# Optimization experiments

Hardware: AMD Instinct MI355X
Metric: run time of the kernel (lower is better)

The kernel has to match this reference:

```python
import jax, jax.numpy as jnp
import numpy as np

B, MAX_NODE, MEM_LEN, DIM, HEADS, LAYERS, DEG = 32, 1024, 256, 128, 4, 4, 16
CH = DIM // HEADS


def setup_inputs() -> dict:
    key = jax.random.key(0)
    ks = jax.random.split(key, 16)
    counts = np.array([512 + 16 * i for i in range(B)])  # ragged graph sizes, sum = 24320
    N = int(counts.sum())
    node2batch = np.repeat(np.arange(B), counts)
    node2pos = np.concatenate([np.arange(c) for c in counts])
    bmask = np.arange(MAX_NODE)[None, :] < counts[:, None]
    rng = np.random.default_rng(0)
    srcs, dsts, off = [], [], 0
    for c in counts:  # edges stay within each graph
        srcs.append(off + rng.integers(0, c, size=DEG * c))
        dsts.append(off + rng.integers(0, c, size=DEG * c))
        off += c
    edge_index = np.stack([np.concatenate(srcs), np.concatenate(dsts)])

    def rn(k, shape, scale=0.05):
        return jax.random.normal(k, shape, jnp.float32) * scale

    return dict(
        node_feats=rn(ks[0], (N, DIM), 1.0),
        edge_feats=rn(ks[1], (edge_index.shape[1], DIM), 1.0),
        memory=rn(ks[2], (B, MEM_LEN, DIM), 1.0),
        Wn=rn(ks[3], (LAYERS, DIM, DIM)), bn=jnp.zeros((LAYERS, DIM)),
        We=rn(ks[4], (LAYERS, DIM, DIM)),
        att_src=rn(ks[5], (LAYERS, HEADS, CH)),
        att_dst=rn(ks[6], (LAYERS, HEADS, CH)),
        att_edge=rn(ks[7], (LAYERS, HEADS, CH)),
        ln1_g=jnp.ones((LAYERS, DIM)), ln1_b=jnp.zeros((LAYERS, DIM)),
        ln2_g=jnp.ones((LAYERS, DIM)), ln2_b=jnp.zeros((LAYERS, DIM)),
        Wq=rn(ks[8], (LAYERS, DIM, DIM)), Wk=rn(ks[9], (LAYERS, DIM, DIM)),
        Wv=rn(ks[10], (LAYERS, DIM, DIM)), Wo=rn(ks[11], (LAYERS, DIM, DIM)),
        Ew1=rn(ks[12], (LAYERS, 3 * DIM, DIM)), Eb1=jnp.zeros((LAYERS, DIM)),
        Ew2=rn(ks[13], (LAYERS, DIM, DIM)), Eb2=jnp.zeros((LAYERS, DIM)),
        edge_index=jnp.asarray(edge_index, jnp.int32),
        node2batch=jnp.asarray(node2batch, jnp.int32),
        node2pos=jnp.asarray(node2pos, jnp.int32),
        batch_mask=jnp.asarray(bmask),
        mem_pad_mask=jnp.ones((B, MEM_LEN), bool),
    )


def _ln(x, g, b):
    mu = x.mean(-1, keepdims=True)
    v = ((x - mu) ** 2).mean(-1, keepdims=True)
    return (x - mu) * jax.lax.rsqrt(v + 1e-5) * g + b


def reference(node_feats, edge_feats, memory, Wn, bn, We, att_src, att_dst, att_edge,
              ln1_g, ln1_b, ln2_g, ln2_b, Wq, Wk, Wv, Wo, Ew1, Eb1, Ew2, Eb2,
              edge_index, node2batch, node2pos, batch_mask, mem_pad_mask):
    N = node_feats.shape[0]
    src, dst = edge_index[0], edge_index[1]
    # [B, max_node, mem_len]: attend only valid memory slots from valid nodes
    cross_mask = mem_pad_mask[:, None, :] & batch_mask[:, :, None]
    x, e = node_feats, edge_feats
    for l in range(LAYERS):
        # --- edge-conditioned GAT conv (segment softmax over dst) ---
        h = (x @ Wn[l]).reshape(N, HEADS, CH)
        eh = (e @ We[l]).reshape(-1, HEADS, CH)
        logits = (h[src] * att_src[l]).sum(-1) + (h[dst] * att_dst[l]).sum(-1) + (eh * att_edge[l]).sum(-1)
        logits = jax.nn.leaky_relu(logits, 0.2)  # [E, H]
        m = jax.ops.segment_max(logits, dst, num_segments=N)
        ew = jnp.exp(logits - m[dst])
        den = jax.ops.segment_sum(ew, dst, num_segments=N)
        alpha = ew / (den[dst] + 1e-16)
        conv = jax.ops.segment_sum(alpha[..., None] * (h[src] + eh), dst, num_segments=N)
        conv = conv.reshape(N, DIM) + bn[l]
        x = jax.nn.relu(_ln(conv, ln1_g[l], ln1_b[l])) + x
        # --- graph2batch scatter into dense padded tensor ---
        dense = jnp.zeros((B, MAX_NODE, DIM), x.dtype).at[node2batch, node2pos].set(x)
        # --- cross attention against memory ---
        q = (dense @ Wq[l]).reshape(B, MAX_NODE, HEADS, CH)
        k = (memory @ Wk[l]).reshape(B, MEM_LEN, HEADS, CH)
        v = (memory @ Wv[l]).reshape(B, MEM_LEN, HEADS, CH)
        scores = jnp.einsum('bqhc,bkhc->bhqk', q, k) / np.float32(np.sqrt(CH))
        scores = jnp.where(cross_mask[:, None], scores, jnp.float32(-1e9))
        ao = jnp.einsum('bhqk,bkhc->bqhc', jax.nn.softmax(scores, axis=-1), v)
        ao = ao.reshape(B, MAX_NODE, DIM) @ Wo[l]
        dense = jax.nn.relu(_ln(ao + dense, ln2_g[l], ln2_b[l]))
        x = dense[node2batch, node2pos]  # batch2graph gather
        # --- residual sparse edge update ---
        ecat = jnp.concatenate([e, x[src], x[dst]], axis=-1)
        e = e + jax.nn.relu(ecat @ Ew1[l] + Eb1[l]) @ Ew2[l] + Eb2[l]
    return x, e
```

## Files before the change

kernel.cpp:

```cpp
#include <hip/hip_runtime.h>

#define DIM    128
#define HEADS  4
#define CH     32
#define MEMLEN 256
#define LAYERS 4

typedef unsigned int uint;
typedef unsigned short ushort;
using bf16x8 = __attribute__((ext_vector_type(8))) short;
using f32x4  = __attribute__((ext_vector_type(4))) float;

__device__ __forceinline__ ushort bf16_rn(float x) {
    uint u = __float_as_uint(x);
    uint r = (u + 0x7fffu + ((u >> 16) & 1u)) >> 16;
    return (ushort)r;
}
__device__ __forceinline__ void split_bf(float v, ushort& h, ushort& lo) {
    h = bf16_rn(v);
    float hf = __uint_as_float(((uint)h) << 16);
    lo = bf16_rn(v - hf);
}


__global__ void copy_f4(const float4* __restrict__ in, float4* __restrict__ out, long n) {
    long i = (long)blockIdx.x * blockDim.x + threadIdx.x;
    long stride = (long)gridDim.x * blockDim.x;
    for (; i < n; i += stride) out[i] = in[i];
}

__global__ void hist_k(const int* __restrict__ dst, int E, int* __restrict__ deg) {
    int e = blockIdx.x * blockDim.x + threadIdx.x;
    if (e < E) atomicAdd(&deg[dst[e]], 1);
}

__global__ void csr_offsets(const int* __restrict__ deg, int n, int* __restrict__ off) {
    __shared__ int part[1024];
    int t = threadIdx.x;
    int chunk = (n + 1023) >> 10;
    int lo = t * chunk, hi = min(lo + chunk, n);
    int s = 0;
    for (int i = lo; i < hi; i++) s += deg[i];
    part[t] = s; __syncthreads();
    for (int d = 1; d < 1024; d <<= 1) {
        int v = part[t];
        int add = (t >= d) ? part[t - d] : 0;
        __syncthreads();
        part[t] = v + add;
        __syncthreads();
    }
    int run = (t == 0) ? 0 : part[t - 1];
    for (int i = lo; i < hi; i++) { off[i] = run; run += deg[i]; }
    if (t == 1023) off[n] = part[1023];
}

__global__ void csr_fill(const int* __restrict__ dst, int E, const int* __restrict__ off,
                         int* __restrict__ cur, int* __restrict__ csr) {
    int e = blockIdx.x * blockDim.x + threadIdx.x;
    if (e < E) {
        int d = dst[e];
        int p = atomicAdd(&cur[d], 1);
        csr[off[d] + p] = e;
    }
}

__global__ void make_w1f(const float* __restrict__ Ew1, ushort* __restrict__ W1f) {
    int i = blockIdx.x * 256 + threadIdx.x;
    if (i >= LAYERS * 12 * 8 * 64 * 8) return;
    int l = i / 49152; int r = i % 49152;
    int ks = r / 4096;  int r2 = r % 4096;
    int ct = r2 / 512;  int r3 = r2 % 512;
    int lane = r3 / 8;  int j = r3 % 8;
    int k = ks * 32 + (lane >> 4) * 8 + j;
    int n = (lane & 15) + 16 * ct;
    const float* W = Ew1 + (size_t)l * 3 * DIM * DIM;
    float v = W[(size_t)(k % 128) * DIM + n];
    ushort h = bf16_rn(v);
    ushort out = h;
    if (k >= 256) {
        float hf = __uint_as_float(((uint)h) << 16);
        out = bf16_rn(v - hf);
    }
    W1f[i] = out;
}

__global__ void make_w2f(const float* __restrict__ Ew2, ushort* __restrict__ W2f) {
    int i = blockIdx.x * 256 + threadIdx.x;
    if (i >= LAYERS * 8 * 8 * 64 * 8) return;
    int l = i / 32768; int r = i % 32768;
    int ks = r / 4096;  int r2 = r % 4096;
    int ct = r2 / 512;  int r3 = r2 % 512;
    int lane = r3 / 8;  int j = r3 % 8;
    int k = ks * 32 + (lane >> 4) * 8 + j;
    int n = (lane & 15) + 16 * ct;
    const float* W = Ew2 + (size_t)l * DIM * DIM;
    W2f[i] = bf16_rn(W[(size_t)(k >> 1) * DIM + n]);
}

__global__ __launch_bounds__(256) void gemm128(const float* __restrict__ A,
                                               const float* __restrict__ W,
                                               const float* __restrict__ bias,
                                               float* __restrict__ out, int R) {
    int r0 = blockIdx.x * 64, t = threadIdx.x;
    __shared__ float at[64][DIM];
    for (int i = t; i < 64 * 32; i += 256) {
        int rr = i >> 5, cc = i & 31;
        if (r0 + rr < R)
            ((float4*)at[rr])[cc] = ((const float4*)(A + (size_t)(r0 + rr) * DIM))[cc];
    }
    __syncthreads();
    int c0 = (t & 31) * 4;
    int rb = (t >> 5) * 8;
    float acc[8][4];
#pragma unroll
    for (int ee = 0; ee < 8; ee++)
        acc[ee][0] = acc[ee][1] = acc[ee][2] = acc[ee][3] = 0.f;
    for (int k = 0; k < DIM; k += 4) {
        float4 w0 = *(const float4*)&W[(k + 0) * DIM + c0];
        float4 w1 = *(const float4*)&W[(k + 1) * DIM + c0];
        float4 w2 = *(const float4*)&W[(k + 2) * DIM + c0];
        float4 w3 = *(const float4*)&W[(k + 3) * DIM + c0];
#pragma unroll
        for (int ee = 0; ee < 8; ee++) {
            float4 a = *(float4*)&at[rb + ee][k];
            acc[ee][0] += a.x * w0.x + a.y * w1.x + a.z * w2.x + a.w * w3.x;
            acc[ee][1] += a.x * w0.y + a.y * w1.y + a.z * w2.y + a.w * w3.y;
            acc[ee][2] += a.x * w0.z + a.y * w1.z + a.z * w2.z + a.w * w3.z;
            acc[ee][3] += a.x * w0.w + a.y * w1.w + a.z * w2.w + a.w * w3.w;
        }
    }
    float4 bb = make_float4(0.f, 0.f, 0.f, 0.f);
    if (bias) bb = *(const float4*)&bias[c0];
#pragma unroll
    for (int ee = 0; ee < 8; ee++) {
        int r = r0 + rb + ee;
        if (r < R) {
            float4 o = make_float4(acc[ee][0] + bb.x, acc[ee][1] + bb.y,
                                   acc[ee][2] + bb.z, acc[ee][3] + bb.w);
            *(float4*)&out[(size_t)r * DIM + c0] = o;
        }
    }
}

__global__ __launch_bounds__(256, 2) void gemm128_dual(const float* __restrict__ A,
                                                       const float* __restrict__ Wa,
                                                       const float* __restrict__ Wb,
                                                       const float* __restrict__ biasA,
                                                       float* __restrict__ outA,
                                                       float* __restrict__ outB, int R) {
    int r0 = blockIdx.x * 64, t = threadIdx.x;
    __shared__ float at[64][DIM];
    for (int i = t; i < 64 * 32; i += 256) {
        int rr = i >> 5, cc = i & 31;
        if (r0 + rr < R)
            ((float4*)at[rr])[cc] = ((const float4*)(A + (size_t)(r0 + rr) * DIM))[cc];
    }
    __syncthreads();
    int c0 = (t & 31) * 4;
    int rb = (t >> 5) * 8;
    float accA[8][4], accB[8][4];
#pragma unroll
    for (int ee = 0; ee < 8; ee++)
#pragma unroll
        for (int j = 0; j < 4; j++) { accA[ee][j] = 0.f; accB[ee][j] = 0.f; }
    for (int k = 0; k < DIM; k += 4) {
        float4 wa0 = *(const float4*)&Wa[(k + 0) * DIM + c0];
        float4 wa1 = *(const float4*)&Wa[(k + 1) * DIM + c0];
        float4 wa2 = *(const float4*)&Wa[(k + 2) * DIM + c0];
        float4 wa3 = *(const float4*)&Wa[(k + 3) * DIM + c0];
        float4 wb0 = *(const float4*)&Wb[(k + 0) * DIM + c0];
        float4 wb1 = *(const float4*)&Wb[(k + 1) * DIM + c0];
        float4 wb2 = *(const float4*)&Wb[(k + 2) * DIM + c0];
        float4 wb3 = *(const float4*)&Wb[(k + 3) * DIM + c0];
#pragma unroll
        for (int ee = 0; ee < 8; ee++) {
            float4 a = *(float4*)&at[rb + ee][k];
            accA[ee][0] += a.x * wa0.x + a.y * wa1.x + a.z * wa2.x + a.w * wa3.x;
            accA[ee][1] += a.x * wa0.y + a.y * wa1.y + a.z * wa2.y + a.w * wa3.y;
            accA[ee][2] += a.x * wa0.z + a.y * wa1.z + a.z * wa2.z + a.w * wa3.z;
            accA[ee][3] += a.x * wa0.w + a.y * wa1.w + a.z * wa2.w + a.w * wa3.w;
            accB[ee][0] += a.x * wb0.x + a.y * wb1.x + a.z * wb2.x + a.w * wb3.x;
            accB[ee][1] += a.x * wb0.y + a.y * wb1.y + a.z * wb2.y + a.w * wb3.y;
            accB[ee][2] += a.x * wb0.z + a.y * wb1.z + a.z * wb2.z + a.w * wb3.z;
            accB[ee][3] += a.x * wb0.w + a.y * wb1.w + a.z * wb2.w + a.w * wb3.w;
        }
    }
    float4 bb = make_float4(0.f, 0.f, 0.f, 0.f);
    if (biasA) bb = *(const float4*)&biasA[c0];
#pragma unroll
    for (int ee = 0; ee < 8; ee++) {
        int r = r0 + rb + ee;
        if (r < R) {
            *(float4*)&outA[(size_t)r * DIM + c0] =
                make_float4(accA[ee][0] + bb.x, accA[ee][1] + bb.y,
                            accA[ee][2] + bb.z, accA[ee][3] + bb.w);
            *(float4*)&outB[(size_t)r * DIM + c0] =
                make_float4(accB[ee][0], accB[ee][1], accB[ee][2], accB[ee][3]);
        }
    }
}

__global__ __launch_bounds__(256) void node_proj_tile(
    const float* __restrict__ x, const float* __restrict__ W,
    const float* __restrict__ att_s, const float* __restrict__ att_d,
    float* __restrict__ h, float* __restrict__ ssrc, float* __restrict__ sdst, int N) {
    int r0 = blockIdx.x * 64, t = threadIdx.x;
    __shared__ float at[64][DIM];
    for (int i = t; i < 64 * 32; i += 256) {
        int rr = i >> 5, cc = i & 31;
        if (r0 + rr < N)
            ((float4*)at[rr])[cc] = ((const float4*)(x + (size_t)(r0 + rr) * DIM))[cc];
    }
    __syncthreads();
    int c0 = (t & 31) * 4;
    int rb = (t >> 5) * 8;
    float acc[8][4];
#pragma unroll
    for (int ee = 0; ee < 8; ee++)
        acc[ee][0] = acc[ee][1] = acc[ee][2] = acc[ee][3] = 0.f;
    for (int k = 0; k < DIM; k += 4) {
        float4 w0 = *(const float4*)&W[(k + 0) * DIM + c0];
        float4 w1 = *(const float4*)&W[(k + 1) * DIM + c0];
        float4 w2 = *(const float4*)&W[(k + 2) * DIM + c0];
        float4 w3 = *(const float4*)&W[(k + 3) * DIM + c0];
#pragma unroll
        for (int ee = 0; ee < 8; ee++) {
            float4 a = *(float4*)&at[rb + ee][k];
            acc[ee][0] += a.x * w0.x + a.y * w1.x + a.z * w2.x + a.w * w3.x;
            acc[ee][1] += a.x * w0.y + a.y * w1.y + a.z * w2.y + a.w * w3.y;
            acc[ee][2] += a.x * w0.z + a.y * w1.z + a.z * w2.z + a.w * w3.z;
            acc[ee][3] += a.x * w0.w + a.y * w1.w + a.z * w2.w + a.w * w3.w;
        }
    }
    int hh = (t & 31) >> 3;
    float4 as = *(const float4*)&att_s[c0];
    float4 ad = *(const float4*)&att_d[c0];
#pragma unroll
    for (int ee = 0; ee < 8; ee++) {
        int r = r0 + rb + ee;
        if (r < N) {
            *(float4*)&h[(size_t)r * DIM + c0] =
                make_float4(acc[ee][0], acc[ee][1], acc[ee][2], acc[ee][3]);
            float ps = acc[ee][0]*as.x + acc[ee][1]*as.y + acc[ee][2]*as.z + acc[ee][3]*as.w;
            float pd = acc[ee][0]*ad.x + acc[ee][1]*ad.y + acc[ee][2]*ad.z + acc[ee][3]*ad.w;
#pragma unroll
            for (int mk = 1; mk < 8; mk <<= 1) {
                ps += __shfl_xor(ps, mk, 32);
                pd += __shfl_xor(pd, mk, 32);
            }
            if (((t & 31) & 7) == 0) {
                ssrc[r * HEADS + hh] = ps;
                sdst[r * HEADS + hh] = pd;
            }
        }
    }
}


__global__ void make_waE(const float* __restrict__ We, const float* __restrict__ att_e,
                         float* __restrict__ waE) {
    int k = threadIdx.x;
#pragma unroll
    for (int h = 0; h < HEADS; h++) {
        float s = 0.f;
#pragma unroll
        for (int c = 0; c < CH; c++) s += We[k * DIM + h * CH + c] * att_e[h * CH + c];
        waE[k * HEADS + h] = s;
    }
}

__global__ void sedge_logits(const float* __restrict__ e, const float* __restrict__ waE,
                             const float* __restrict__ ssrc, const float* __restrict__ sdst,
                             const int* __restrict__ src, const int* __restrict__ dst,
                             float* __restrict__ lw, int E) {
    __shared__ float w[DIM * HEADS];
    int t = threadIdx.x;
    w[t] = waE[t]; w[t + 256] = waE[t + 256];
    __syncthreads();
    int g = t >> 5, lane = t & 31;
    int eid = blockIdx.x * 8 + g;
    if (eid >= E) return;
    const float* er = e + (size_t)eid * DIM;
    float s0 = 0.f, s1 = 0.f, s2 = 0.f, s3 = 0.f;
#pragma unroll
    for (int j = 0; j < 4; j++) {
        int k = lane + 32 * j;
        float v = er[k];
        s0 += v * w[k * 4 + 0]; s1 += v * w[k * 4 + 1];
        s2 += v * w[k * 4 + 2]; s3 += v * w[k * 4 + 3];
    }
#pragma unroll
    for (int m = 16; m; m >>= 1) {
        s0 += __shfl_xor(s0, m, 32); s1 += __shfl_xor(s1, m, 32);
        s2 += __shfl_xor(s2, m, 32); s3 += __shfl_xor(s3, m, 32);
    }
    if (lane == 0) {
        int sn = src[eid] * HEADS, dn = dst[eid] * HEADS;
        float l0 = ssrc[sn + 0] + sdst[dn + 0] + s0;
        float l1 = ssrc[sn + 1] + sdst[dn + 1] + s1;
        float l2 = ssrc[sn + 2] + sdst[dn + 2] + s2;
        float l3 = ssrc[sn + 3] + sdst[dn + 3] + s3;
        lw[eid * 4 + 0] = (l0 >= 0.f) ? l0 : 0.2f * l0;
        lw[eid * 4 + 1] = (l1 >= 0.f) ? l1 : 0.2f * l1;
        lw[eid * 4 + 2] = (l2 >= 0.f) ? l2 : 0.2f * l2;
        lw[eid * 4 + 3] = (l3 >= 0.f) ? l3 : 0.2f * l3;
    }
}

__global__ void seg_softmax(const int* __restrict__ off, const int* __restrict__ csr,
                            float* __restrict__ lw, float* __restrict__ den, int NH) {
    int i = blockIdx.x * blockDim.x + threadIdx.x;
    if (i >= NH) return;
    int n = i >> 2, hh = i & 3;
    int o0 = off[n], o1 = off[n + 1];
    float m = -1e30f;
    for (int o = o0; o < o1; o++) m = fmaxf(m, lw[csr[o] * HEADS + hh]);
    float s = 0.f;
    for (int o = o0; o < o1; o++) {
        int idx = csr[o] * HEADS + hh;
        float w = __expf(lw[idx] - m);
        lw[idx] = w;
        s += w;
    }
    den[i] = s;
}

__global__ __launch_bounds__(512) void conv_ln4(
    const int* __restrict__ off, const int* __restrict__ csr, const int* __restrict__ src,
    const float* __restrict__ lw, const float* __restrict__ den,
    const float* __restrict__ hbuf, const float* __restrict__ e, const float* __restrict__ We,
    const float* __restrict__ bn, const float* __restrict__ g, const float* __restrict__ b,
    float* __restrict__ x, int N) {
    int t = threadIdx.x;
    int tt = t & 127, part = t >> 7;
    int n = blockIdx.x;
    int hh = tt >> 5;
    __shared__ float aggeP[4][HEADS][DIM];
    __shared__ float acchP[4][DIM];
    __shared__ float ehcP[4][DIM];
    __shared__ float wred[16];
    int o0 = off[n], o1 = off[n + 1];
    float acch = 0.f, a0 = 0.f, a1 = 0.f, a2 = 0.f, a3 = 0.f;
    for (int o = o0 + part; o < o1; o += 4) {
        int eid = csr[o];
        int s = src[eid];
        float4 al = *(const float4*)&lw[eid * 4];
        acch += ((&al.x)[hh]) * hbuf[(size_t)s * DIM + tt];
        float ev = e[(size_t)eid * DIM + tt];
        a0 += al.x * ev; a1 += al.y * ev; a2 += al.z * ev; a3 += al.w * ev;
    }
    aggeP[part][0][tt] = a0; aggeP[part][1][tt] = a1;
    aggeP[part][2][tt] = a2; aggeP[part][3][tt] = a3;
    acchP[part][tt] = acch;
    __syncthreads();
    float ehc = 0.f;
    int k0 = part * 32;
    for (int k = k0; k < k0 + 32; k++) {
        float ag = aggeP[0][hh][k] + aggeP[1][hh][k] + aggeP[2][hh][k] + aggeP[3][hh][k];
        ehc += ag * We[k * DIM + tt];
    }
    ehcP[part][tt] = ehc;
    __syncthreads();
    float conv = (acchP[0][tt] + acchP[1][tt] + acchP[2][tt] + acchP[3][tt]
                + ehcP[0][tt] + ehcP[1][tt] + ehcP[2][tt] + ehcP[3][tt])
                 / (den[n * HEADS + hh] + 1e-16f) + bn[tt];
    int w = t >> 6;
    float s1 = conv;
#pragma unroll
    for (int mk = 32; mk; mk >>= 1) s1 += __shfl_xor(s1, mk, 64);
    if ((t & 63) == 0) wred[w] = s1;
    __syncthreads();
    float mu = (wred[w] + wred[w ^ 1]) * (1.f / DIM);
    float diff = conv - mu;
    float s2 = diff * diff;
#pragma unroll
    for (int mk = 32; mk; mk >>= 1) s2 += __shfl_xor(s2, mk, 64);
    if ((t & 63) == 0) wred[8 + w] = s2;
    __syncthreads();
    float var = (wred[8 + w] + wred[8 + (w ^ 1)]) * (1.f / DIM);
    if (part == 0) {
        float y = diff * rsqrtf(var + 1e-5f) * g[tt] + b[tt];
        x[(size_t)n * DIM + tt] = fmaxf(y, 0.f) + x[(size_t)n * DIM + tt];
    }
}

__global__ __launch_bounds__(256) void cross_attn_tile(
    float* __restrict__ x, const float* __restrict__ qg,
    const float* __restrict__ kb, const float* __restrict__ vb,
    const float* __restrict__ Wo, const float* __restrict__ g,
    const float* __restrict__ b, const int* __restrict__ boff) {
    int bb = blockIdx.y;
    int n0 = boff[bb] + blockIdx.x * 64;
    int cnt = boff[bb + 1] - n0;
    if (cnt <= 0) return;
    int nq = min(64, cnt);
    int t = threadIdx.x;
    int q = t & 63, h = t >> 6;

    __shared__ float smem[64 * 132];

    float qv[32];
    if (q < nq) {
        const float4* qp = (const float4*)(qg + (size_t)(n0 + q) * DIM + h * CH);
#pragma unroll
        for (int j = 0; j < 8; j++) {
            float4 v = qp[j];
            qv[4*j+0] = v.x; qv[4*j+1] = v.y; qv[4*j+2] = v.z; qv[4*j+3] = v.w;
        }
    } else {
#pragma unroll
        for (int c = 0; c < 32; c++) qv[c] = 0.f;
    }

    float oacc[32];
#pragma unroll
    for (int c = 0; c < 32; c++) oacc[c] = 0.f;
    float m = -1e30f, l = 0.f;

    const float4* Ksrc = (const float4*)(kb + (size_t)bb * MEMLEN * DIM);
    const float4* Vsrc = (const float4*)(vb + (size_t)bb * MEMLEN * DIM);
    float4* Kl = (float4*)smem;
    float4* Vl = (float4*)(smem + 32 * DIM);

    for (int ch = 0; ch < MEMLEN / 32; ch++) {
        __syncthreads();
#pragma unroll
        for (int r = 0; r < 4; r++) {
            int idx = t + r * 256;
            Kl[idx] = Ksrc[ch * 1024 + idx];
            Vl[idx] = Vsrc[ch * 1024 + idx];
        }
        __syncthreads();
        float sc[32];
#pragma unroll
        for (int kk = 0; kk < 32; kk++) {
            const float* kp = smem + kk * DIM + h * CH;
            float s = 0.f;
#pragma unroll
            for (int c = 0; c < 32; c++) s += qv[c] * kp[c];
            sc[kk] = s * 0.17677669529663689f;
        }
        float mc = sc[0];
#pragma unroll
        for (int kk = 1; kk < 32; kk++) mc = fmaxf(mc, sc[kk]);
        float mn = fmaxf(m, mc);
        float scale = __expf(m - mn);
        m = mn;
        float ls = 0.f;
#pragma unroll
        for (int kk = 0; kk < 32; kk++) {
            float w = __expf(sc[kk] - mn);
            sc[kk] = w;
            ls += w;
        }
        l = l * scale + ls;
#pragma unroll
        for (int c = 0; c < 32; c++) oacc[c] *= scale;
#pragma unroll
        for (int kk = 0; kk < 32; kk++) {
            const float* vp = smem + 32 * DIM + kk * DIM + h * CH;
            float w = sc[kk];
#pragma unroll
            for (int c = 0; c < 32; c++) oacc[c] += w * vp[c];
        }
    }
    __syncthreads();
    {
        float inv = 1.f / l;
        float* ap = smem + q * 132 + h * CH;
#pragma unroll
        for (int c = 0; c < 32; c++) ap[c] = oacc[c] * inv;
    }
    __syncthreads();
    int c0 = (t & 31) * 4;
    int rb = (t >> 5) * 8;
    float acc2[8][4];
#pragma unroll
    for (int ee = 0; ee < 8; ee++)
        acc2[ee][0] = acc2[ee][1] = acc2[ee][2] = acc2[ee][3] = 0.f;
    for (int k = 0; k < DIM; k += 4) {
        float4 w0 = *(const float4*)&Wo[(k + 0) * DIM + c0];
        float4 w1 = *(const float4*)&Wo[(k + 1) * DIM + c0];
        float4 w2 = *(const float4*)&Wo[(k + 2) * DIM + c0];
        float4 w3 = *(const float4*)&Wo[(k + 3) * DIM + c0];
#pragma unroll
        for (int ee = 0; ee < 8; ee++) {
            float4 a = *(const float4*)(smem + (rb + ee) * 132 + k);
            acc2[ee][0] += a.x * w0.x + a.y * w1.x + a.z * w2.x + a.w * w3.x;
            acc2[ee][1] += a.x * w0.y + a.y * w1.y + a.z * w2.y + a.w * w3.y;
            acc2[ee][2] += a.x * w0.z + a.y * w1.z + a.z * w2.z + a.w * w3.z;
            acc2[ee][3] += a.x * w0.w + a.y * w1.w + a.z * w2.w + a.w * w3.w;
        }
    }
    float4 gg = *(const float4*)&g[c0];
    float4 bb4 = *(const float4*)&b[c0];
#pragma unroll
    for (int ee = 0; ee < 8; ee++) {
        int r = rb + ee;
        if (r < nq) {
            float4 xr = *(const float4*)&x[(size_t)(n0 + r) * DIM + c0];
            float o0 = acc2[ee][0] + xr.x, o1 = acc2[ee][1] + xr.y;
            float o2 = acc2[ee][2] + xr.z, o3 = acc2[ee][3] + xr.w;
            float s1 = o0 + o1 + o2 + o3;
#pragma unroll
            for (int mk = 16; mk; mk >>= 1) s1 += __shfl_xor(s1, mk, 32);
            float mu = s1 * (1.f / DIM);
            float d0 = o0 - mu, d1 = o1 - mu, d2 = o2 - mu, d3 = o3 - mu;
            float s2 = d0*d0 + d1*d1 + d2*d2 + d3*d3;
#pragma unroll
            for (int mk = 16; mk; mk >>= 1) s2 += __shfl_xor(s2, mk, 32);
            float rs = rsqrtf(s2 * (1.f / DIM) + 1e-5f);
            float4 o = make_float4(fmaxf(d0 * rs * gg.x + bb4.x, 0.f),
                                   fmaxf(d1 * rs * gg.y + bb4.y, 0.f),
                                   fmaxf(d2 * rs * gg.z + bb4.z, 0.f),
                                   fmaxf(d3 * rs * gg.w + bb4.w, 0.f));
            *(float4*)&x[(size_t)(n0 + r) * DIM + c0] = o;
        }
    }
}

__global__ __launch_bounds__(256) void edge_mlp_mfma(
    float* __restrict__ e, const float* __restrict__ xs, const float* __restrict__ xd,
    const int* __restrict__ src, const int* __restrict__ dst,
    const ushort* __restrict__ W1f,
    const ushort* __restrict__ W2f,
    const float* __restrict__ Eb2, int E) {
    __shared__ ushort As[64 * 256];
    __shared__ ushort Bs[2][4096];
    int t = threadIdx.x;
    int e0 = blockIdx.x * 64;

#pragma unroll
    for (int it = 0; it < 8; it++) {
        int i = t + it * 256;
        int row = i >> 5, c4 = i & 31;
        float4 v;
        if (e0 + row < E) v = *(const float4*)&e[(size_t)(e0 + row) * DIM + c4 * 4];
        else v = make_float4(0.f, 0.f, 0.f, 0.f);
        ushort h0, l0, h1, l1, h2, l2, h3, l3;
        split_bf(v.x, h0, l0); split_bf(v.y, h1, l1);
        split_bf(v.z, h2, l2); split_bf(v.w, h3, l3);
        int k = c4 * 4;
        int off = k & 7;
        int kbh = (k >> 3) ^ (row & 7);
        int kbl = ((128 + k) >> 3) ^ (row & 7);
        uint2 hw, lw2;
        hw.x = (uint)h0 | ((uint)h1 << 16); hw.y = (uint)h2 | ((uint)h3 << 16);
        lw2.x = (uint)l0 | ((uint)l1 << 16); lw2.y = (uint)l2 | ((uint)l3 << 16);
        *(uint2*)&As[row * 256 + kbh * 8 + off] = hw;
        *(uint2*)&As[row * 256 + kbl * 8 + off] = lw2;
    }

    auto loadB = [&](const ushort* Wf, int ks, uint4& p0, uint4& p1) {
        const ushort* s = Wf + (size_t)ks * 4096;
        p0 = *(const uint4*)&s[t * 8];
        p1 = *(const uint4*)&s[(t + 256) * 8];
    };
    auto writeB = [&](int buf, const uint4& p0, const uint4& p1) {
        *(uint4*)&Bs[buf][t * 8] = p0;
        *(uint4*)&Bs[buf][(t + 256) * 8] = p1;
    };

    {
        uint4 p0, p1;
        loadB(W1f, 0, p0, p1);
        writeB(0, p0, p1);
    }
    __syncthreads();

    int l = t & 63, wid = t >> 6;
    int rowbase = wid * 16;
    int arow = rowbase + (l & 15);
    int g = l >> 4;
    int swz = arow & 7;

    f32x4 acc[8];
#pragma unroll
    for (int ct = 0; ct < 8; ct++) acc[ct] = (f32x4){0.f, 0.f, 0.f, 0.f};

    for (int ks = 0; ks < 12; ks++) {
        int buf = ks & 1;
        uint4 p0, p1;
        bool havepf = (ks + 1) < 12;
        if (havepf) loadB(W1f, ks + 1, p0, p1);
        int ksA = (ks < 8) ? ks : (ks - 8);
        int kbm = (ksA * 4 + g) ^ swz;
        bf16x8 af = *(bf16x8*)&As[arow * 256 + kbm * 8];
#pragma unroll
        for (int ct = 0; ct < 8; ct++) {
            bf16x8 bfrag = *(bf16x8*)&Bs[buf][(ct * 64 + l) * 8];
            acc[ct] = __builtin_amdgcn_mfma_f32_16x16x32_bf16(af, bfrag, acc[ct], 0, 0, 0);
        }
        __syncthreads();
        if (havepf) writeB(buf ^ 1, p0, p1);
        __syncthreads();
    }

    int srow[4], drow[4], grow4[4];
#pragma unroll
    for (int j = 0; j < 4; j++) {
        int grow = e0 + rowbase + g * 4 + j;
        grow4[j] = grow;
        if (grow < E) { srow[j] = src[grow]; drow[j] = dst[grow]; }
        else { srow[j] = 0; drow[j] = 0; }
    }
#pragma unroll
    for (int ct = 0; ct < 8; ct++) {
        int col = (l & 15) + 16 * ct;
        int kb = col >> 2;
        int off = (2 * col) & 7;
#pragma unroll
        for (int j = 0; j < 4; j++) {
            float v = acc[ct][j];
            if (grow4[j] < E)
                v += xs[(size_t)srow[j] * DIM + col] + xd[(size_t)drow[j] * DIM + col];
            v = fmaxf(v, 0.f);
            ushort h, lo;
            split_bf(v, h, lo);
            int rowloc = rowbase + g * 4 + j;
            int kbm = kb ^ (rowloc & 7);
            *(uint*)&As[rowloc * 256 + kbm * 8 + off] = (uint)h | ((uint)lo << 16);
        }
    }
    {
        uint4 p0, p1;
        loadB(W2f, 0, p0, p1);
        __syncthreads();
        writeB(0, p0, p1);
    }
    __syncthreads();

    f32x4 acc2[8];
#pragma unroll
    for (int ct = 0; ct < 8; ct++) acc2[ct] = (f32x4){0.f, 0.f, 0.f, 0.f};
    for (int ks = 0; ks < 8; ks++) {
        int buf = ks & 1;
        uint4 p0, p1;
        bool havepf = (ks + 1) < 8;
        if (havepf) loadB(W2f, ks + 1, p0, p1);
        int kbm = (ks * 4 + g) ^ swz;
        bf16x8 af = *(bf16x8*)&As[arow * 256 + kbm * 8];
#pragma unroll
        for (int ct = 0; ct < 8; ct++) {
            bf16x8 bfrag = *(bf16x8*)&Bs[buf][(ct * 64 + l) * 8];
            acc2[ct] = __builtin_amdgcn_mfma_f32_16x16x32_bf16(af, bfrag, acc2[ct], 0, 0, 0);
        }
        __syncthreads();
        if (havepf) writeB(buf ^ 1, p0, p1);
        __syncthreads();
    }

#pragma unroll
    for (int ct = 0; ct < 8; ct++) {
        int col = (l & 15) + 16 * ct;
        float b2 = Eb2[col];
#pragma unroll
        for (int j = 0; j < 4; j++) {
            if (grow4[j] < E) {
                size_t idx = (size_t)grow4[j] * DIM + col;
                e[idx] += acc2[ct][j] + b2;
            }
        }
    }
}


extern "C" void kernel_launch(void* const* d_in, const int* in_sizes, int n_in,
                              void* d_out, int out_size, void* d_ws, size_t ws_size,
                              hipStream_t stream) {
    const float* node_feats = (const float*)d_in[0];
    const float* edge_feats = (const float*)d_in[1];
    const float* memory     = (const float*)d_in[2];
    const float* Wn   = (const float*)d_in[3];
    const float* bn   = (const float*)d_in[4];
    const float* We   = (const float*)d_in[5];
    const float* att_src  = (const float*)d_in[6];
    const float* att_dst  = (const float*)d_in[7];
    const float* att_edge = (const float*)d_in[8];
    const float* ln1_g = (const float*)d_in[9];
    const float* ln1_b = (const float*)d_in[10];
    const float* ln2_g = (const float*)d_in[11];
    const float* ln2_b = (const float*)d_in[12];
    const float* Wq = (const float*)d_in[13];
    const float* Wk = (const float*)d_in[14];
    const float* Wv = (const float*)d_in[15];
    const float* Wo = (const float*)d_in[16];
    const float* Ew1 = (const float*)d_in[17];
    const float* Eb1 = (const float*)d_in[18];
    const float* Ew2 = (const float*)d_in[19];
    const float* Eb2 = (const float*)d_in[20];
    const int* edge_index = (const int*)d_in[21];
    const int* node2batch = (const int*)d_in[22];

    const int N = in_sizes[0] / DIM;
    const int E = in_sizes[1] / DIM;
    const int Bn = in_sizes[2] / (MEMLEN * DIM);
    const int* srcA = edge_index;
    const int* dstA = edge_index + E;

    float* x = (float*)d_out;
    float* e = x + (size_t)N * DIM;

    char* p = (char*)d_ws;
    auto carve = [&](size_t bytes) {
        void* r = (void*)p;
        p += (bytes + 255) & ~(size_t)255;
        return r;
    };
    float* h     = (float*)carve((size_t)N * DIM * 4);
    float* qg    = (float*)carve((size_t)N * DIM * 4);
    float* xs    = (float*)carve((size_t)N * DIM * 4);
    float* xd    = (float*)carve((size_t)N * DIM * 4);
    float* ssrc  = (float*)carve((size_t)N * HEADS * 4);
    float* sdst  = (float*)carve((size_t)N * HEADS * 4);
    float* lw    = (float*)carve((size_t)E * HEADS * 4);
    float* den   = (float*)carve((size_t)N * HEADS * 4);
    float* waE   = (float*)carve((size_t)DIM * HEADS * 4);
    float* kbuf  = (float*)carve((size_t)Bn * MEMLEN * DIM * 4);
    float* vbuf  = (float*)carve((size_t)Bn * MEMLEN * DIM * 4);
    ushort* W1f  = (ushort*)carve((size_t)LAYERS * 12 * 4096 * 2);
    ushort* W2f  = (ushort*)carve((size_t)LAYERS * 8 * 4096 * 2);
    int* deg     = (int*)carve((size_t)N * 4);
    int* cur     = (int*)carve((size_t)N * 4);
    int* off     = (int*)carve(((size_t)N + 1) * 4);
    int* csr     = (int*)carve((size_t)E * 4);
    int* bcnt    = (int*)carve((size_t)Bn * 4);
    int* boff    = (int*)carve(((size_t)Bn + 1) * 4);

    {
        long nx = (long)N * DIM / 4;
        copy_f4<<<dim3(2048), dim3(256), 0, stream>>>((const float4*)node_feats, (float4*)x, nx);
        long nen = (long)E * DIM / 4;
        copy_f4<<<dim3(4096), dim3(256), 0, stream>>>((const float4*)edge_feats, (float4*)e, nen);
    }

    make_w1f<<<dim3((LAYERS * 49152 + 255) / 256), dim3(256), 0, stream>>>(Ew1, W1f);
    make_w2f<<<dim3((LAYERS * 32768 + 255) / 256), dim3(256), 0, stream>>>(Ew2, W2f);

    hipMemsetAsync(deg, 0, (size_t)N * 4, stream);
    hipMemsetAsync(cur, 0, (size_t)N * 4, stream);
    hipMemsetAsync(bcnt, 0, (size_t)Bn * 4, stream);
    hist_k<<<dim3((E + 255) / 256), dim3(256), 0, stream>>>(dstA, E, deg);
    csr_offsets<<<dim3(1), dim3(1024), 0, stream>>>(deg, N, off);
    csr_fill<<<dim3((E + 255) / 256), dim3(256), 0, stream>>>(dstA, E, off, cur, csr);
    hist_k<<<dim3((N + 255) / 256), dim3(256), 0, stream>>>(node2batch, N, bcnt);
    csr_offsets<<<dim3(1), dim3(1024), 0, stream>>>(bcnt, Bn, boff);

    const int mrows = Bn * MEMLEN;
    const int maxTiles = 1024 / 64;
    for (int l = 0; l < LAYERS; l++) {
        const float* Wn_l  = Wn  + (size_t)l * DIM * DIM;
        const float* We_l  = We  + (size_t)l * DIM * DIM;
        const float* Wq_l  = Wq  + (size_t)l * DIM * DIM;
        const float* Wo_l  = Wo  + (size_t)l * DIM * DIM;
        const float* Wk_l  = Wk  + (size_t)l * DIM * DIM;
        const float* Wv_l  = Wv  + (size_t)l * DIM * DIM;
        const float* Ew1_l = Ew1 + (size_t)l * 3 * DIM * DIM;

        node_proj_tile<<<dim3((N + 63) / 64), dim3(256), 0, stream>>>(
            x, Wn_l, att_src + l * DIM, att_dst + l * DIM, h, ssrc, sdst, N);
        make_waE<<<dim3(1), dim3(DIM), 0, stream>>>(We_l, att_edge + l * DIM, waE);
        sedge_logits<<<dim3((E + 7) / 8), dim3(256), 0, stream>>>(
            e, waE, ssrc, sdst, srcA, dstA, lw, E);
        seg_softmax<<<dim3((N * HEADS + 255) / 256), dim3(256), 0, stream>>>(
            off, csr, lw, den, N * HEADS);
        conv_ln4<<<dim3(N), dim3(512), 0, stream>>>(
            off, csr, srcA, lw, den, h, e, We_l,
            bn + l * DIM, ln1_g + l * DIM, ln1_b + l * DIM, x, N);
        gemm128_dual<<<dim3((mrows + 63) / 64), dim3(256), 0, stream>>>(
            memory, Wk_l, Wv_l, nullptr, kbuf, vbuf, mrows);
        gemm128<<<dim3((N + 63) / 64), dim3(256), 0, stream>>>(
            x, Wq_l, nullptr, qg, N);
        cross_attn_tile<<<dim3(maxTiles, Bn), dim3(256), 0, stream>>>(
            x, qg, kbuf, vbuf, Wo_l, ln2_g + l * DIM, ln2_b + l * DIM, boff);
        gemm128_dual<<<dim3((N + 63) / 64), dim3(256), 0, stream>>>(
            x, Ew1_l + (size_t)DIM * DIM, Ew1_l + (size_t)2 * DIM * DIM,
            Eb1 + l * DIM, xs, xd, N);
        edge_mlp_mfma<<<dim3((E + 63) / 64), dim3(256), 0, stream>>>(
            e, xs, xd, srcA, dstA,
            W1f + (size_t)l * 12 * 4096, W2f + (size_t)l * 8 * 4096,
            Eb2 + l * DIM, E);
    }
}
```

Before: 3.856 ms.

## Keep edge-MLP weight fragments in registers and split waves by output columns

The edge MLP kernel no longer stages W1/W2 tiles through a double-buffered shared-memory buffer with two barriers per k-step. Each wave now owns two 16-column output tiles across all 64 rows and loads its weight fragments straight from global memory into registers. Only the A operand stays in LDS, and a launch-bounds hint of two blocks per CU is added. This removes the per-step barriers and the LDS traffic for B, in exchange for four times more A-fragment LDS reads per wave and high register pressure from the held fragments, which could cause spills or lower occupancy.

```diff
diff --git a/kernel.cpp b/kernel.cpp
--- a/kernel.cpp
+++ b/kernel.cpp
@@ -519,14 +519,13 @@
     }
 }
 
-__global__ __launch_bounds__(256) void edge_mlp_mfma(
+__global__ __launch_bounds__(256, 2) void edge_mlp_mfma(
     float* __restrict__ e, const float* __restrict__ xs, const float* __restrict__ xd,
     const int* __restrict__ src, const int* __restrict__ dst,
     const ushort* __restrict__ W1f,
     const ushort* __restrict__ W2f,
     const float* __restrict__ Eb2, int E) {
     __shared__ ushort As[64 * 256];
-    __shared__ ushort Bs[2][4096];
     int t = threadIdx.x;
     int e0 = blockIdx.x * 64;
 
@@ -551,114 +550,100 @@
         *(uint2*)&As[row * 256 + kbl * 8 + off] = lw2;
     }
 
-    auto loadB = [&](const ushort* Wf, int ks, uint4& p0, uint4& p1) {
-        const ushort* s = Wf + (size_t)ks * 4096;
-        p0 = *(const uint4*)&s[t * 8];
-        p1 = *(const uint4*)&s[(t + 256) * 8];
-    };
-    auto writeB = [&](int buf, const uint4& p0, const uint4& p1) {
-        *(uint4*)&Bs[buf][t * 8] = p0;
-        *(uint4*)&Bs[buf][(t + 256) * 8] = p1;
-    };
-
-    {
-        uint4 p0, p1;
-        loadB(W1f, 0, p0, p1);
-        writeB(0, p0, p1);
-    }
-    __syncthreads();
-
     int l = t & 63, wid = t >> 6;
-    int rowbase = wid * 16;
-    int arow = rowbase + (l & 15);
     int g = l >> 4;
-    int swz = arow & 7;
-
-    f32x4 acc[8];
-#pragma unroll
-    for (int ct = 0; ct < 8; ct++) acc[ct] = (f32x4){0.f, 0.f, 0.f, 0.f};
-
+    int lr = l & 15;
+    int ct0 = 2 * wid, ct1 = 2 * wid + 1;
+
+    bf16x8 b1[12][2];
+#pragma unroll
     for (int ks = 0; ks < 12; ks++) {
-        int buf = ks & 1;
-        uint4 p0, p1;
-        bool havepf = (ks + 1) < 12;
-        if (havepf) loadB(W1f, ks + 1, p0, p1);
+        b1[ks][0] = *(const bf16x8*)&W1f[(size_t)ks * 4096 + ct0 * 512 + l * 8];
+        b1[ks][1] = *(const bf16x8*)&W1f[(size_t)ks * 4096 + ct1 * 512 + l * 8];
+    }
+
+    __syncthreads();
+
+    f32x4 acc[4][2];
+#pragma unroll
+    for (int r = 0; r < 4; r++) {
+        acc[r][0] = (f32x4){0.f, 0.f, 0.f, 0.f};
+        acc[r][1] = (f32x4){0.f, 0.f, 0.f, 0.f};
+    }
+
+#pragma unroll
+    for (int ks = 0; ks < 12; ks++) {
         int ksA = (ks < 8) ? ks : (ks - 8);
-        int kbm = (ksA * 4 + g) ^ swz;
-        bf16x8 af = *(bf16x8*)&As[arow * 256 + kbm * 8];
-#pragma unroll
-        for (int ct = 0; ct < 8; ct++) {
-            bf16x8 bfrag = *(bf16x8*)&Bs[buf][(ct * 64 + l) * 8];
-            acc[ct] = __builtin_amdgcn_mfma_f32_16x16x32_bf16(af, bfrag, acc[ct], 0, 0, 0);
-        }
-        __syncthreads();
-        if (havepf) writeB(buf ^ 1, p0, p1);
-        __syncthreads();
-    }
-
-    int srow[4], drow[4], grow4[4];
-#pragma unroll
-    for (int j = 0; j < 4; j++) {
-        int grow = e0 + rowbase + g * 4 + j;
-        grow4[j] = grow;
-        if (grow < E) { srow[j] = src[grow]; drow[j] = dst[grow]; }
-        else { srow[j] = 0; drow[j] = 0; }
-    }
-#pragma unroll
-    for (int ct = 0; ct < 8; ct++) {
-        int col = (l & 15) + 16 * ct;
-        int kb = col >> 2;
-        int off = (2 * col) & 7;
+#pragma unroll
+        for (int r = 0; r < 4; r++) {
+            int arow = r * 16 + lr;
+            int kbm = (ksA * 4 + g) ^ (arow & 7);
+            bf16x8 af = *(bf16x8*)&As[arow * 256 + kbm * 8];
+            acc[r][0] = __builtin_amdgcn_mfma_f32_16x16x32_bf16(af, b1[ks][0], acc[r][0], 0, 0, 0);
+            acc[r][1] = __builtin_amdgcn_mfma_f32_16x16x32_bf16(af, b1[ks][1], acc[r][1], 0, 0, 0);
+        }
+    }
+
+    bf16x8 b2f[8][2];
+#pragma unroll
+    for (int ks = 0; ks < 8; ks++) {
+        b2f[ks][0] = *(const bf16x8*)&W2f[(size_t)ks * 4096 + ct0 * 512 + l * 8];
+        b2f[ks][1] = *(const bf16x8*)&W2f[(size_t)ks * 4096 + ct1 * 512 + l * 8];
+    }
+
+    int col0 = lr + 16 * ct0, col1 = lr + 16 * ct1;
+    int kb0 = col0 >> 2, off0 = (2 * col0) & 7;
+    int kb1 = col1 >> 2, off1 = (2 * col1) & 7;
+#pragma unroll
+    for (int r = 0; r < 4; r++) {
 #pragma unroll
         for (int j = 0; j < 4; j++) {
-            float v = acc[ct][j];
-            if (grow4[j] < E)
-                v += xs[(size_t)srow[j] * DIM + col] + xd[(size_t)drow[j] * DIM + col];
-            v = fmaxf(v, 0.f);
-            ushort h, lo;
-            split_bf(v, h, lo);
-            int rowloc = rowbase + g * 4 + j;
-            int kbm = kb ^ (rowloc & 7);
-            *(uint*)&As[rowloc * 256 + kbm * 8 + off] = (uint)h | ((uint)lo << 16);
-        }
-    }
-    {
-        uint4 p0, p1;
-        loadB(W2f, 0, p0, p1);
-        __syncthreads();
-        writeB(0, p0, p1);
-    }
-    __syncthreads();
-
-    f32x4 acc2[8];
-#pragma unroll
-    for (int ct = 0; ct < 8; ct++) acc2[ct] = (f32x4){0.f, 0.f, 0.f, 0.f};
+            int rowloc = r * 16 + g * 4 + j;
+            int grow = e0 + rowloc;
+            float v0 = acc[r][0][j], v1 = acc[r][1][j];
+            if (grow < E) {
+                int s = src[grow], d = dst[grow];
+                v0 += xs[(size_t)s * DIM + col0] + xd[(size_t)d * DIM + col0];
+                v1 += xs[(size_t)s * DIM + col1] + xd[(size_t)d * DIM + col1];
+            }
+            v0 = fmaxf(v0, 0.f); v1 = fmaxf(v1, 0.f);
+            ushort h0s, l0s, h1s, l1s;
+            split_bf(v0, h0s, l0s);
+            split_bf(v1, h1s, l1s);
+            int rs = rowloc & 7;
+            *(uint*)&As[rowloc * 256 + (kb0 ^ rs) * 8 + off0] = (uint)h0s | ((uint)l0s << 16);
+            *(uint*)&As[rowloc * 256 + (kb1 ^ rs) * 8 + off1] = (uint)h1s | ((uint)l1s << 16);
+        }
+    }
+    __syncthreads();
+
+    f32x4 acc2[4][2];
+#pragma unroll
+    for (int r = 0; r < 4; r++) {
+        acc2[r][0] = (f32x4){0.f, 0.f, 0.f, 0.f};
+        acc2[r][1] = (f32x4){0.f, 0.f, 0.f, 0.f};
+    }
+#pragma unroll
     for (int ks = 0; ks < 8; ks++) {
-        int buf = ks & 1;
-        uint4 p0, p1;
-        bool havepf = (ks + 1) < 8;
-        if (havepf) loadB(W2f, ks + 1, p0, p1);
-        int kbm = (ks * 4 + g) ^ swz;
-        bf16x8 af = *(bf16x8*)&As[arow * 256 + kbm * 8];
-#pragma unroll
-        for (int ct = 0; ct < 8; ct++) {
-            bf16x8 bfrag = *(bf16x8*)&Bs[buf][(ct * 64 + l) * 8];
-            acc2[ct] = __builtin_amdgcn_mfma_f32_16x16x32_bf16(af, bfrag, acc2[ct], 0, 0, 0);
-        }
-        __syncthreads();
-        if (havepf) writeB(buf ^ 1, p0, p1);
-        __syncthreads();
-    }
-
-#pragma unroll
-    for (int ct = 0; ct < 8; ct++) {
-        int col = (l & 15) + 16 * ct;
-        float b2 = Eb2[col];
+#pragma unroll
+        for (int r = 0; r < 4; r++) {
+            int arow = r * 16 + lr;
+            int kbm = (ks * 4 + g) ^ (arow & 7);
+            bf16x8 af = *(bf16x8*)&As[arow * 256 + kbm * 8];
+            acc2[r][0] = __builtin_amdgcn_mfma_f32_16x16x32_bf16(af, b2f[ks][0], acc2[r][0], 0, 0, 0);
+            acc2[r][1] = __builtin_amdgcn_mfma_f32_16x16x32_bf16(af, b2f[ks][1], acc2[r][1], 0, 0, 0);
+        }
+    }
+
+    float b20 = Eb2[col0], b21 = Eb2[col1];
+#pragma unroll
+    for (int r = 0; r < 4; r++) {
 #pragma unroll
         for (int j = 0; j < 4; j++) {
-            if (grow4[j] < E) {
-                size_t idx = (size_t)grow4[j] * DIM + col;
-                e[idx] += acc2[ct][j] + b2;
+            int grow = e0 + r * 16 + g * 4 + j;
+            if (grow < E) {
+                e[(size_t)grow * DIM + col0] += acc2[r][0][j] + b20;
+                e[(size_t)grow * DIM + col1] += acc2[r][1][j] + b21;
             }
         }
     }
```

Result: no change. 3.915 ms (+1.5%).
